# Kernel optimization log

Hardware: AMD Instinct MI355X
Metric: run time of the kernel (lower is better)

Reference implementation:

```python
import jax, jax.numpy as jnp
import numpy as np

HID = 3072
HEADS = 24
HD = HID // HEADS  # 128
MLP = 4 * HID      # 12288
B, L, TXT = 1, 2304, 256
EPS_LN = 1e-6
EPS_RMS = 1e-6


def setup_inputs() -> dict:
    key = jax.random.key(0)
    ks = jax.random.split(key, 12)
    s = 0.02
    return {
        "hidden_states": jax.random.normal(ks[0], (B, L, HID), jnp.float32),
        "temb": jax.random.normal(ks[1], (B, HID), jnp.float32),
        "cos": jax.random.normal(ks[2], (L - TXT, HD), jnp.float32),
        "sin": jax.random.normal(ks[3], (L - TXT, HD), jnp.float32),
        "ada_w": jax.random.normal(ks[4], (HID, 3 * HID), jnp.float32) * s,
        "ada_b": jnp.zeros((3 * HID,), jnp.float32),
        "lin1_w": jax.random.normal(ks[5], (HID, 3 * HID + MLP), jnp.float32) * s,
        "lin1_b": jnp.zeros((3 * HID + MLP,), jnp.float32),
        "lin2_w": jax.random.normal(ks[6], (HID + MLP, HID), jnp.float32) * s,
        "lin2_b": jnp.zeros((HID,), jnp.float32),
        "qn_w": jnp.ones((HD,), jnp.float32),
        "kn_w": jnp.ones((HD,), jnp.float32),
        "txt_len": TXT,
    }


def _rotate_half(x):
    # interleaved pairs: (x0,x1) -> (-x1, x0)
    xr = x[..., 0::2]
    xi = x[..., 1::2]
    return jnp.stack([-xi, xr], axis=-1).reshape(x.shape)


def _rms_norm(x, w):
    var = jnp.mean(jnp.square(x), axis=-1, keepdims=True)
    return x * jax.lax.rsqrt(var + EPS_RMS) * w


def reference(hidden_states, temb, cos, sin, ada_w, ada_b, lin1_w, lin1_b,
              lin2_w, lin2_b, qn_w, kn_w, txt_len):
    # AdaLayerNormZeroSingle
    emb = jax.nn.silu(temb) @ ada_w + ada_b               # [B, 3*HID]
    shift, scale, gate = jnp.split(emb, 3, axis=-1)
    mu = jnp.mean(hidden_states, axis=-1, keepdims=True)
    var = jnp.var(hidden_states, axis=-1, keepdims=True)
    ln = (hidden_states - mu) * jax.lax.rsqrt(var + EPS_LN)
    norm_x = ln * (1.0 + scale[:, None, :]) + shift[:, None, :]

    # fused qkv + mlp-in projection
    proj = norm_x @ lin1_w + lin1_b                       # [B, L, 3*HID+MLP]
    qkv, mlp = proj[..., : 3 * HID], proj[..., 3 * HID:]
    qkv = qkv.reshape(B, L, 3, HEADS, HD)
    q, k, v = qkv[:, :, 0], qkv[:, :, 1], qkv[:, :, 2]    # [B, L, H, D]

    q = _rms_norm(q, qn_w)
    k = _rms_norm(k, kn_w)

    # RoPE on image tokens only (first L - txt_len)
    img = L - txt_len
    c = cos[None, :, None, :]
    s = sin[None, :, None, :]
    q_img = q[:, :img] * c + _rotate_half(q[:, :img]) * s
    k_img = k[:, :img] * c + _rotate_half(k[:, :img]) * s
    q = jnp.concatenate([q_img, q[:, img:]], axis=1)
    k = jnp.concatenate([k_img, k[:, img:]], axis=1)

    # SDPA (full, non-causal)
    scale_a = 1.0 / jnp.sqrt(jnp.asarray(HD, q.dtype))
    scores = jnp.einsum("blhd,bmhd->bhlm", q, k) * scale_a
    probs = jax.nn.softmax(scores, axis=-1)
    attn = jnp.einsum("bhlm,bmhd->blhd", probs, v).reshape(B, L, HID)

    # gated parallel-MLP output
    out = jnp.concatenate([attn, jax.nn.gelu(mlp, approximate=True)], axis=-1)
    out = out @ lin2_w + lin2_b
    return hidden_states + out * gate[:, None, :]
```

## Files before the change

kernel.cpp:

```cpp
#include <hip/hip_runtime.h>
#include <stdint.h>

#define HID   3072
#define LSEQ  2304
#define NH    24
#define HD    128
#define N1    21504
#define QKVW  9216
#define X2W   15360

typedef __bf16 bf16x8 __attribute__((ext_vector_type(8)));
typedef unsigned short u16x8 __attribute__((ext_vector_type(8)));
typedef float f32x4 __attribute__((ext_vector_type(4)));

#define MFMA(a,b,c) __builtin_amdgcn_mfma_f32_16x16x32_bf16((a),(b),(c),0,0,0)

#define GLOAD_LDS16(g, l) __builtin_amdgcn_global_load_lds( \
    (const __attribute__((address_space(1))) unsigned int*)(g), \
    (__attribute__((address_space(3))) unsigned int*)(l), 16, 0, 0)

__device__ __forceinline__ unsigned short f2b(float f){
  unsigned int u = __builtin_bit_cast(unsigned int, f);
  u += 0x7fffu + ((u >> 16) & 1u);
  return (unsigned short)(u >> 16);
}
__device__ __forceinline__ float b2f(unsigned short b){
  return __builtin_bit_cast(float, ((unsigned int)b) << 16);
}
__device__ __forceinline__ unsigned int pk2(float lo, float hi){
  return (unsigned int)f2b(lo) | ((unsigned int)f2b(hi) << 16);
}

__global__ void silu_k(const float* __restrict__ temb, float* __restrict__ st){
  int i = blockIdx.x*256 + threadIdx.x;
  if (i < HID){ float x = temb[i]; st[i] = x / (1.f + __expf(-x)); }
}

__global__ __launch_bounds__(256) void ada_k(const float* __restrict__ st,
                                             const float* __restrict__ aw,
                                             const float* __restrict__ ab,
                                             float* __restrict__ emb){
  int c = threadIdx.x & 31, g = threadIdx.x >> 5;
  int col = blockIdx.x*32 + c;
  float acc = 0.f;
  for (int k = g; k < HID; k += 8)
    acc += st[k] * aw[(size_t)k*QKVW + col];
  __shared__ float part[256];
  part[threadIdx.x] = acc;
  __syncthreads();
  if (threadIdx.x < 32){
    float s = 0.f;
    #pragma unroll
    for (int j = 0; j < 8; ++j) s += part[j*32 + threadIdx.x];
    int cc = blockIdx.x*32 + threadIdx.x;
    emb[cc] = s + ab[cc];
  }
}

__global__ __launch_bounds__(256) void ln_k(const float* __restrict__ hs,
                                            const float* __restrict__ emb,
                                            unsigned short* __restrict__ nx){
  int l = blockIdx.x, t = threadIdx.x;
  const float* row = hs + (size_t)l*HID;
  float x[12], s = 0.f, ss = 0.f;
  #pragma unroll
  for (int i = 0; i < 12; ++i){ x[i] = row[t + i*256]; s += x[i]; ss += x[i]*x[i]; }
  #pragma unroll
  for (int off = 32; off; off >>= 1){ s += __shfl_xor(s, off); ss += __shfl_xor(ss, off); }
  __shared__ float red[8];
  int w = t >> 6, lane = t & 63;
  if (!lane){ red[w] = s; red[4+w] = ss; }
  __syncthreads();
  s = red[0]+red[1]+red[2]+red[3];
  ss = red[4]+red[5]+red[6]+red[7];
  float mu = s * (1.f/HID);
  float var = ss * (1.f/HID) - mu*mu;
  float rstd = rsqrtf(var + 1e-6f);
  #pragma unroll
  for (int i = 0; i < 12; ++i){
    int c = t + i*256;
    float v = (x[i]-mu)*rstd*(1.f + emb[HID + c]) + emb[c];
    nx[(size_t)l*HID + c] = f2b(v);
  }
}

__global__ __launch_bounds__(256) void tconv_k(const float* __restrict__ W,
                                               unsigned short* __restrict__ WT,
                                               int ldw, int K){
  __shared__ unsigned short Ls[64*66];
  int k0 = blockIdx.x*64, n0 = blockIdx.y*64;
  int t = threadIdx.x;
  #pragma unroll
  for (int p = 0; p < 4; ++p){
    int idx = p*256 + t, row = idx >> 4, c4 = idx & 15;
    float4 f = *(const float4*)(W + (size_t)(k0+row)*ldw + n0 + c4*4);
    *(unsigned int*)&Ls[row*66 + c4*4]     = pk2(f.x, f.y);
    *(unsigned int*)&Ls[row*66 + c4*4 + 2] = pk2(f.z, f.w);
  }
  __syncthreads();
  #pragma unroll
  for (int p = 0; p < 2; ++p){
    int idx = p*256 + t, n = idx >> 3, ch = idx & 7;
    u16x8 r;
    #pragma unroll
    for (int j = 0; j < 8; ++j) r[j] = Ls[(ch*8 + j)*66 + n];
    *(uint4*)(WT + (size_t)(n0+n)*K + k0 + ch*8) = __builtin_bit_cast(uint4, r);
  }
}

template<int EPI>
__global__ __launch_bounds__(512, 2)
void gemm256_k(const unsigned short* __restrict__ A, const unsigned short* __restrict__ BT,
               const float* __restrict__ bias, int K, int NT,
               unsigned short* __restrict__ o16)
{
  __shared__ __align__(16) unsigned short As[4][256*32];
  __shared__ __align__(16) unsigned short Bs[4][256*32];
  const int t = threadIdx.x;
  const int m0 = blockIdx.y * 256, n0 = blockIdx.x * 256;
  const int w = t >> 6, lane = t & 63, quad = lane >> 4, l16 = lane & 15;
  const int wr = w >> 2, wc = w & 3;

  const unsigned short* aSrc[2];
  const unsigned short* bSrc[2];
  #pragma unroll
  for (int p = 0; p < 2; ++p){
    int lin = p*512 + t;
    int row = lin >> 2;
    int ch  = (lin & 3) ^ ((row >> 1) & 3);
    aSrc[p] = A  + (size_t)(m0 + row)*K + ch*8;
    bSrc[p] = BT + (size_t)(n0 + row)*K + ch*8;
  }
  const int ldsOff0 = w*512;
  const int ldsOff1 = 4096 + w*512;

#define STAGE_A(slot, pf) do{ \
    GLOAD_LDS16(aSrc[0] + (size_t)(pf)*32, &As[slot][ldsOff0]); \
    GLOAD_LDS16(aSrc[1] + (size_t)(pf)*32, &As[slot][ldsOff1]); }while(0)
#define STAGE_B(slot, pf) do{ \
    GLOAD_LDS16(bSrc[0] + (size_t)(pf)*32, &Bs[slot][ldsOff0]); \
    GLOAD_LDS16(bSrc[1] + (size_t)(pf)*32, &Bs[slot][ldsOff1]); }while(0)

  const int kSwz  = (quad ^ ((l16 >> 1) & 3)) * 8;
  const int aBase = (wr*128 + l16)*32 + kSwz;
  const int bBase = (wc*64  + l16)*32 + kSwz;

  f32x4 acc[8][4];
  #pragma unroll
  for (int i = 0; i < 8; ++i)
    #pragma unroll
    for (int j = 0; j < 4; ++j) acc[i][j] = (f32x4){0.f,0.f,0.f,0.f};

  STAGE_A(0, 0); STAGE_B(0, 0);
  STAGE_A(1, 1); STAGE_B(1, 1);
  STAGE_A(2, 2); STAGE_B(2, 2);
  asm volatile("s_waitcnt vmcnt(8)" ::: "memory");
  __builtin_amdgcn_sched_barrier(0);
  __builtin_amdgcn_s_barrier();

  for (int kt = 0; kt < NT; ++kt){
    const int slot  = kt & 3;
    const int wslot = (kt + 3) & 3;
    const int pf    = (kt + 3 < NT) ? (kt + 3) : (NT - 1);
    bf16x8 af[4], bf[4];

    STAGE_A(wslot, pf);
    #pragma unroll
    for (int i = 0; i < 4; ++i)
      af[i] = __builtin_bit_cast(bf16x8, *(const uint4*)&As[slot][aBase + i*512]);
    #pragma unroll
    for (int i = 0; i < 4; ++i)
      bf[i] = __builtin_bit_cast(bf16x8, *(const uint4*)&Bs[slot][bBase + i*512]);
    __builtin_amdgcn_s_barrier();
    asm volatile("s_waitcnt lgkmcnt(0)" ::: "memory");
    __builtin_amdgcn_sched_barrier(0);
    __builtin_amdgcn_s_setprio(1);
    #pragma unroll
    for (int mi = 0; mi < 4; ++mi)
      #pragma unroll
      for (int ni = 0; ni < 4; ++ni)
        acc[mi][ni] = MFMA(af[mi], bf[ni], acc[mi][ni]);
    __builtin_amdgcn_s_setprio(0);

    STAGE_B(wslot, pf);
    #pragma unroll
    for (int i = 0; i < 4; ++i)
      af[i] = __builtin_bit_cast(bf16x8, *(const uint4*)&As[slot][aBase + 2048 + i*512]);
    __builtin_amdgcn_s_barrier();
    asm volatile("s_waitcnt lgkmcnt(0)" ::: "memory");
    __builtin_amdgcn_sched_barrier(0);
    __builtin_amdgcn_s_setprio(1);
    #pragma unroll
    for (int mi = 0; mi < 4; ++mi)
      #pragma unroll
      for (int ni = 0; ni < 4; ++ni)
        acc[4+mi][ni] = MFMA(af[mi], bf[ni], acc[4+mi][ni]);
    __builtin_amdgcn_s_setprio(0);
    asm volatile("s_waitcnt vmcnt(8)" ::: "memory");
    __builtin_amdgcn_sched_barrier(0);
    __builtin_amdgcn_s_barrier();
  }
#undef STAGE_A
#undef STAGE_B

  asm volatile("s_waitcnt vmcnt(0)" ::: "memory");

  #pragma unroll
  for (int mi = 0; mi < 8; ++mi){
    #pragma unroll
    for (int ni = 0; ni < 4; ++ni){
      const int gn = n0 + wc*64 + ni*16 + l16;
      const float bs = bias[gn];
      #pragma unroll
      for (int r = 0; r < 4; ++r){
        const int gm = m0 + wr*128 + mi*16 + quad*4 + r;
        float v = acc[mi][ni][r] + bs;
        if (EPI == 1){
          o16[(size_t)gm*QKVW + gn] = f2b(v);
        } else {
          float e = __expf(1.5957691216057308f*(v + 0.044715f*v*v*v));
          float th = 1.f - 2.f/(e + 1.f);
          o16[(size_t)gm*X2W + HID + gn] = f2b(0.5f*v*(1.f + th));
        }
      }
    }
  }
}

template<int EPI>
__global__ __launch_bounds__(256)
void gemm_k(const unsigned short* __restrict__ A, const unsigned short* __restrict__ BT,
            const float* __restrict__ bias, int K,
            unsigned short* __restrict__ o16, float* __restrict__ of,
            const float* __restrict__ hid, const float* __restrict__ emb)
{
  __shared__ __align__(16) unsigned short As[128*32];
  __shared__ __align__(16) unsigned short Bs[128*32];
  const int t = threadIdx.x;
  const int m0 = blockIdx.y * 128, n0 = blockIdx.x * 128;
  const int w = t >> 6, lane = t & 63, quad = lane >> 4, l16 = lane & 15;
  const int wm = w >> 1, wn = w & 1;

  f32x4 acc[4][4];
  #pragma unroll
  for (int i = 0; i < 4; ++i)
    #pragma unroll
    for (int j = 0; j < 4; ++j) acc[i][j] = (f32x4){0.f,0.f,0.f,0.f};

  const unsigned short* aG = A  + (size_t)(m0 + w*32 + (lane>>2))*K + (lane&3)*8;
  const unsigned short* bG = BT + (size_t)(n0 + w*32 + (lane>>2))*K + (lane&3)*8;
  unsigned short* aL = &As[w*1024];
  unsigned short* bL = &Bs[w*1024];

  for (int k0 = 0; k0 < K; k0 += 32){
    __syncthreads();
    GLOAD_LDS16(aG + k0,          aL);
    GLOAD_LDS16(aG + 16*K + k0,   aL + 512);
    GLOAD_LDS16(bG + k0,          bL);
    GLOAD_LDS16(bG + 16*K + k0,   bL + 512);
    __syncthreads();

    bf16x8 af[4], bf[4];
    #pragma unroll
    for (int mt = 0; mt < 4; ++mt)
      af[mt] = __builtin_bit_cast(bf16x8, *(const uint4*)&As[(wm*64 + mt*16 + l16)*32 + quad*8]);
    #pragma unroll
    for (int nt = 0; nt < 4; ++nt)
      bf[nt] = __builtin_bit_cast(bf16x8, *(const uint4*)&Bs[(wn*64 + nt*16 + l16)*32 + quad*8]);
    #pragma unroll
    for (int mt = 0; mt < 4; ++mt)
      #pragma unroll
      for (int nt = 0; nt < 4; ++nt)
        acc[mt][nt] = MFMA(af[mt], bf[nt], acc[mt][nt]);
  }

  #pragma unroll
  for (int mt = 0; mt < 4; ++mt){
    #pragma unroll
    for (int nt = 0; nt < 4; ++nt){
      const int gn = n0 + wn*64 + nt*16 + l16;
      const float bs = bias[gn];
      #pragma unroll
      for (int r = 0; r < 4; ++r){
        const int gm = m0 + wm*64 + mt*16 + quad*4 + r;
        float v = acc[mt][nt][r] + bs;
        if (EPI == 1){
          o16[(size_t)gm*QKVW + gn] = f2b(v);
        } else if (EPI == 3){
          float e = __expf(1.5957691216057308f*(v + 0.044715f*v*v*v));
          float th = 1.f - 2.f/(e + 1.f);
          o16[(size_t)gm*X2W + HID + gn] = f2b(0.5f*v*(1.f + th));
        } else {
          of[(size_t)gm*HID + gn] = hid[(size_t)gm*HID + gn] + v * emb[2*HID + gn];
        }
      }
    }
  }
}

__global__ __launch_bounds__(256) void qknorm_k(unsigned short* __restrict__ qkv,
                                                const float* __restrict__ qn,
                                                const float* __restrict__ kn,
                                                const float* __restrict__ cosp,
                                                const float* __restrict__ sinp,
                                                const int* __restrict__ txtp){
  int img = LSEQ - txtp[0];
  int rid = blockIdx.x*4 + (threadIdx.x >> 6);
  int lane = threadIdx.x & 63;
  int which = rid / (NH*LSEQ);
  int rem   = rid % (NH*LSEQ);
  int h = rem / LSEQ, l = rem % LSEQ;
  unsigned short* p = qkv + (size_t)l*QKVW + which*HID + h*HD + lane*2;
  unsigned int both = *(const unsigned int*)p;
  float x0 = b2f((unsigned short)(both & 0xffffu));
  float x1 = b2f((unsigned short)(both >> 16));
  float ss = x0*x0 + x1*x1;
  #pragma unroll
  for (int off = 32; off; off >>= 1) ss += __shfl_xor(ss, off);
  float r = rsqrtf(ss*(1.f/HD) + 1e-6f);
  const float* wv = which ? kn : qn;
  float y0 = x0*r*wv[lane*2], y1 = x1*r*wv[lane*2+1];
  if (l < img){
    float c0 = cosp[l*HD + lane*2], c1 = cosp[l*HD + lane*2 + 1];
    float s0 = sinp[l*HD + lane*2], s1 = sinp[l*HD + lane*2 + 1];
    float t0 = y0*c0 - y1*s0;
    float t1 = y1*c1 + y0*s1;
    y0 = t0; y1 = t1;
  }
  if (which == 0){ y0 *= 0.08838834764831845f; y1 *= 0.08838834764831845f; }
  *(unsigned int*)p = pk2(y0, y1);
}

__global__ __launch_bounds__(256) void vtrans_k(const unsigned short* __restrict__ qkv,
                                                unsigned short* __restrict__ vT){
  __shared__ __align__(16) unsigned short Ls[64*136];
  int h = blockIdx.y, m0 = blockIdx.x*64, t = threadIdx.x;
  #pragma unroll
  for (int p = 0; p < 4; ++p){
    int lin = p*256 + t, m = lin >> 4, ch = lin & 15;
    *(uint4*)&Ls[m*136 + ch*8] =
      *(const uint4*)(qkv + (size_t)(m0+m)*QKVW + 2*HID + h*HD + ch*8);
  }
  __syncthreads();
  #pragma unroll
  for (int p = 0; p < 4; ++p){
    int lin = p*256 + t, d = lin >> 3, ch = lin & 7;
    u16x8 r;
    #pragma unroll
    for (int j = 0; j < 8; ++j) r[j] = Ls[(ch*8 + j)*136 + d];
    *(uint4*)(vT + (size_t)h*HD*LSEQ + (size_t)d*LSEQ + m0 + ch*8) =
      __builtin_bit_cast(uint4, r);
  }
}

__global__ __launch_bounds__(256)
void attn_k(const unsigned short* __restrict__ qkv,
            const unsigned short* __restrict__ vT,
            unsigned short* __restrict__ x2)
{
  __shared__ __align__(16) unsigned short Ks[32*136];
  __shared__ __align__(16) unsigned short Vt[128*40];
  __shared__ __align__(16) unsigned short Ps[4*16*40];
  const int h = blockIdx.y, qb = blockIdx.x*64;
  const int t = threadIdx.x, w = t >> 6, lane = t & 63, quad = lane >> 4, l16 = lane & 15;

  bf16x8 aq[4];
  {
    const unsigned short* qp = qkv + (size_t)(qb + w*16 + l16)*QKVW + h*HD;
    #pragma unroll
    for (int dt = 0; dt < 4; ++dt)
      aq[dt] = __builtin_bit_cast(bf16x8, *(const uint4*)(qp + dt*32 + quad*8));
  }
  f32x4 o[8];
  #pragma unroll
  for (int i = 0; i < 8; ++i) o[i] = (f32x4){0.f,0.f,0.f,0.f};
  float mr[4] = {-1e30f,-1e30f,-1e30f,-1e30f};
  float lr[4] = {0.f,0.f,0.f,0.f};

  const unsigned short* kb = qkv + HID + h*HD;
  const unsigned short* vb = vT + (size_t)h*HD*LSEQ;
  unsigned short* pw = &Ps[w*16*40];

  for (int m0 = 0; m0 < LSEQ; m0 += 32){
    __syncthreads();
    #pragma unroll
    for (int p = 0; p < 2; ++p){
      int lin = p*256 + t, kr = lin >> 4, ch = lin & 15;
      *(uint4*)&Ks[kr*136 + ch*8] = *(const uint4*)(kb + (size_t)(m0+kr)*QKVW + ch*8);
    }
    #pragma unroll
    for (int p = 0; p < 2; ++p){
      int lin = p*256 + t, d = lin >> 2, ch = lin & 3;
      *(uint4*)&Vt[d*40 + ch*8] = *(const uint4*)(vb + (size_t)d*LSEQ + m0 + ch*8);
    }
    __syncthreads();

    f32x4 s0 = (f32x4){0.f,0.f,0.f,0.f}, s1 = s0;
    #pragma unroll
    for (int dt = 0; dt < 4; ++dt){
      bf16x8 k0 = __builtin_bit_cast(bf16x8, *(const uint4*)&Ks[l16*136 + dt*32 + quad*8]);
      bf16x8 k1 = __builtin_bit_cast(bf16x8, *(const uint4*)&Ks[(16+l16)*136 + dt*32 + quad*8]);
      s0 = MFMA(aq[dt], k0, s0);
      s1 = MFMA(aq[dt], k1, s1);
    }
    #pragma unroll
    for (int r = 0; r < 4; ++r){
      float mx = fmaxf(s0[r], s1[r]);
      mx = fmaxf(mx, __shfl_xor(mx, 1));
      mx = fmaxf(mx, __shfl_xor(mx, 2));
      mx = fmaxf(mx, __shfl_xor(mx, 4));
      mx = fmaxf(mx, __shfl_xor(mx, 8));
      float mn = fmaxf(mr[r], mx);
      float al = __expf(mr[r] - mn);
      float p0 = __expf(s0[r] - mn), p1 = __expf(s1[r] - mn);
      float rs = p0 + p1;
      rs += __shfl_xor(rs, 1);
      rs += __shfl_xor(rs, 2);
      rs += __shfl_xor(rs, 4);
      rs += __shfl_xor(rs, 8);
      lr[r] = lr[r]*al + rs;
      mr[r] = mn;
      #pragma unroll
      for (int i = 0; i < 8; ++i) o[i][r] *= al;
      int q = quad*4 + r;
      pw[q*40 + l16]      = f2b(p0);
      pw[q*40 + 16 + l16] = f2b(p1);
    }
    bf16x8 pa = __builtin_bit_cast(bf16x8, *(const uint4*)&pw[l16*40 + quad*8]);
    #pragma unroll
    for (int i = 0; i < 8; ++i){
      bf16x8 vv = __builtin_bit_cast(bf16x8, *(const uint4*)&Vt[(i*16 + l16)*40 + quad*8]);
      o[i] = MFMA(pa, vv, o[i]);
    }
  }
  #pragma unroll
  for (int i = 0; i < 8; ++i){
    #pragma unroll
    for (int r = 0; r < 4; ++r){
      int q = qb + w*16 + quad*4 + r;
      x2[(size_t)q*X2W + h*HD + i*16 + l16] = f2b(o[i][r] / lr[r]);
    }
  }
}

extern "C" void kernel_launch(void* const* d_in, const int* in_sizes, int n_in,
                              void* d_out, int out_size, void* d_ws, size_t ws_size,
                              hipStream_t stream) {
  const float* hs     = (const float*)d_in[0];
  const float* temb   = (const float*)d_in[1];
  const float* cosp   = (const float*)d_in[2];
  const float* sinp   = (const float*)d_in[3];
  const float* ada_w  = (const float*)d_in[4];
  const float* ada_b  = (const float*)d_in[5];
  const float* lin1_w = (const float*)d_in[6];
  const float* lin1_b = (const float*)d_in[7];
  const float* lin2_w = (const float*)d_in[8];
  const float* lin2_b = (const float*)d_in[9];
  const float* qn     = (const float*)d_in[10];
  const float* kn     = (const float*)d_in[11];
  const int*   txt    = (const int*)d_in[12];
  float* out = (float*)d_out;

  char* ws = (char*)d_ws;
  float*          st  = (float*)ws;
  float*          emb = (float*)(ws + 12288);
  unsigned short* nx  = (unsigned short*)(ws + 49152);
  unsigned short* qkv = (unsigned short*)(ws + 14204928);
  unsigned short* x2  = (unsigned short*)(ws + 56672256);
  unsigned short* vT  = (unsigned short*)(ws + 127451136);
  unsigned short* wt  = (unsigned short*)(ws + 141606912);

  silu_k<<<12, 256, 0, stream>>>(temb, st);
  ada_k<<<288, 256, 0, stream>>>(st, ada_w, ada_b, emb);
  ln_k<<<LSEQ, 256, 0, stream>>>(hs, emb, nx);

  tconv_k<<<dim3(HID/64, QKVW/64), 256, 0, stream>>>(lin1_w, wt, N1, HID);
  gemm256_k<1><<<dim3(QKVW/256, LSEQ/256), 512, 0, stream>>>(nx, wt, lin1_b, HID, HID/32, qkv);
  tconv_k<<<dim3(HID/64, (N1-QKVW)/64), 256, 0, stream>>>(lin1_w + QKVW, wt, N1, HID);
  gemm256_k<3><<<dim3((N1-QKVW)/256, LSEQ/256), 512, 0, stream>>>(nx, wt, lin1_b + QKVW, HID, HID/32, x2);

  qknorm_k<<<(2*NH*LSEQ)/4, 256, 0, stream>>>(qkv, qn, kn, cosp, sinp, txt);
  vtrans_k<<<dim3(LSEQ/64, NH), 256, 0, stream>>>(qkv, vT);
  attn_k<<<dim3(LSEQ/64, NH), 256, 0, stream>>>(qkv, vT, x2);

  tconv_k<<<dim3(X2W/64, HID/64), 256, 0, stream>>>(lin2_w, wt, HID, X2W);
  gemm_k<2><<<dim3(HID/128, LSEQ/128), 256, 0, stream>>>(x2, wt, lin2_b, X2W,
                                                         nullptr, out, hs, emb);
}
```

Measured before the change: 1.901 ms.

## Replace lin2 GEMM with 4-stage pipelined 128x256 tile kernel; add MFMA priority in attention

```diff
diff --git a/kernel.cpp b/kernel.cpp
--- a/kernel.cpp
+++ b/kernel.cpp
@@ -227,19 +227,39 @@
   }
 }
 
-template<int EPI>
-__global__ __launch_bounds__(256)
-void gemm_k(const unsigned short* __restrict__ A, const unsigned short* __restrict__ BT,
-            const float* __restrict__ bias, int K,
-            unsigned short* __restrict__ o16, float* __restrict__ of,
-            const float* __restrict__ hid, const float* __restrict__ emb)
+__global__ __launch_bounds__(512, 2)
+void gemm256n_k(const unsigned short* __restrict__ A, const unsigned short* __restrict__ BT,
+                const float* __restrict__ bias, int K, int NT,
+                float* __restrict__ of, const float* __restrict__ hid,
+                const float* __restrict__ emb)
 {
-  __shared__ __align__(16) unsigned short As[128*32];
-  __shared__ __align__(16) unsigned short Bs[128*32];
+  __shared__ __align__(16) unsigned short As[4][128*32];
+  __shared__ __align__(16) unsigned short Bs[4][256*32];
   const int t = threadIdx.x;
-  const int m0 = blockIdx.y * 128, n0 = blockIdx.x * 128;
+  const int m0 = blockIdx.y * 128, n0 = blockIdx.x * 256;
   const int w = t >> 6, lane = t & 63, quad = lane >> 4, l16 = lane & 15;
-  const int wm = w >> 1, wn = w & 1;
+  const int wr = w >> 2, wc = w & 3;
+
+  const unsigned short* aSrc;
+  { int row = t >> 2, ch = (t & 3) ^ ((row >> 1) & 3);
+    aSrc = A + (size_t)(m0 + row)*K + ch*8; }
+  const unsigned short* bSrc[2];
+  #pragma unroll
+  for (int p = 0; p < 2; ++p){
+    int lin = p*512 + t, row = lin >> 2, ch = (lin & 3) ^ ((row >> 1) & 3);
+    bSrc[p] = BT + (size_t)(n0 + row)*K + ch*8;
+  }
+  const int aOff  = w*512;
+  const int bOff0 = w*512, bOff1 = 4096 + w*512;
+
+#define STAGE(slot, pf) do{ \
+    GLOAD_LDS16(aSrc    + (size_t)(pf)*32, &As[slot][aOff]); \
+    GLOAD_LDS16(bSrc[0] + (size_t)(pf)*32, &Bs[slot][bOff0]); \
+    GLOAD_LDS16(bSrc[1] + (size_t)(pf)*32, &Bs[slot][bOff1]); }while(0)
+
+  const int kSwz  = (quad ^ ((l16 >> 1) & 3)) * 8;
+  const int aBase = (wr*64 + l16)*32 + kSwz;
+  const int bBase = (wc*64 + l16)*32 + kSwz;
 
   f32x4 acc[4][4];
   #pragma unroll
@@ -247,52 +267,53 @@
     #pragma unroll
     for (int j = 0; j < 4; ++j) acc[i][j] = (f32x4){0.f,0.f,0.f,0.f};
 
-  const unsigned short* aG = A  + (size_t)(m0 + w*32 + (lane>>2))*K + (lane&3)*8;
-  const unsigned short* bG = BT + (size_t)(n0 + w*32 + (lane>>2))*K + (lane&3)*8;
-  unsigned short* aL = &As[w*1024];
-  unsigned short* bL = &Bs[w*1024];
-
-  for (int k0 = 0; k0 < K; k0 += 32){
-    __syncthreads();
-    GLOAD_LDS16(aG + k0,          aL);
-    GLOAD_LDS16(aG + 16*K + k0,   aL + 512);
-    GLOAD_LDS16(bG + k0,          bL);
-    GLOAD_LDS16(bG + 16*K + k0,   bL + 512);
-    __syncthreads();
-
+  STAGE(0, 0); STAGE(1, 1); STAGE(2, 2);
+  asm volatile("s_waitcnt vmcnt(6)" ::: "memory");
+  __builtin_amdgcn_sched_barrier(0);
+  __builtin_amdgcn_s_barrier();
+
+  for (int kt = 0; kt < NT; ++kt){
+    const int slot  = kt & 3;
+    const int wslot = (kt + 3) & 3;
+    const int pf    = (kt + 3 < NT) ? (kt + 3) : (NT - 1);
     bf16x8 af[4], bf[4];
-    #pragma unroll
-    for (int mt = 0; mt < 4; ++mt)
-      af[mt] = __builtin_bit_cast(bf16x8, *(const uint4*)&As[(wm*64 + mt*16 + l16)*32 + quad*8]);
-    #pragma unroll
-    for (int nt = 0; nt < 4; ++nt)
-      bf[nt] = __builtin_bit_cast(bf16x8, *(const uint4*)&Bs[(wn*64 + nt*16 + l16)*32 + quad*8]);
-    #pragma unroll
-    for (int mt = 0; mt < 4; ++mt)
+
+    STAGE(wslot, pf);
+    #pragma unroll
+    for (int i = 0; i < 4; ++i)
+      af[i] = __builtin_bit_cast(bf16x8, *(const uint4*)&As[slot][aBase + i*512]);
+    #pragma unroll
+    for (int i = 0; i < 4; ++i)
+      bf[i] = __builtin_bit_cast(bf16x8, *(const uint4*)&Bs[slot][bBase + i*512]);
+    __builtin_amdgcn_s_barrier();
+    asm volatile("s_waitcnt lgkmcnt(0)" ::: "memory");
+    __builtin_amdgcn_sched_barrier(0);
+    __builtin_amdgcn_s_setprio(1);
+    #pragma unroll
+    for (int mi = 0; mi < 4; ++mi)
       #pragma unroll
-      for (int nt = 0; nt < 4; ++nt)
-        acc[mt][nt] = MFMA(af[mt], bf[nt], acc[mt][nt]);
-  }
-
-  #pragma unroll
-  for (int mt = 0; mt < 4; ++mt){
-    #pragma unroll
-    for (int nt = 0; nt < 4; ++nt){
-      const int gn = n0 + wn*64 + nt*16 + l16;
+      for (int ni = 0; ni < 4; ++ni)
+        acc[mi][ni] = MFMA(af[mi], bf[ni], acc[mi][ni]);
+    __builtin_amdgcn_s_setprio(0);
+    asm volatile("s_waitcnt vmcnt(6)" ::: "memory");
+    __builtin_amdgcn_sched_barrier(0);
+    __builtin_amdgcn_s_barrier();
+  }
+#undef STAGE
+
+  asm volatile("s_waitcnt vmcnt(0)" ::: "memory");
+
+  #pragma unroll
+  for (int mi = 0; mi < 4; ++mi){
+    #pragma unroll
+    for (int ni = 0; ni < 4; ++ni){
+      const int gn = n0 + wc*64 + ni*16 + l16;
       const float bs = bias[gn];
       #pragma unroll
       for (int r = 0; r < 4; ++r){
-        const int gm = m0 + wm*64 + mt*16 + quad*4 + r;
-        float v = acc[mt][nt][r] + bs;
-        if (EPI == 1){
-          o16[(size_t)gm*QKVW + gn] = f2b(v);
-        } else if (EPI == 3){
-          float e = __expf(1.5957691216057308f*(v + 0.044715f*v*v*v));
-          float th = 1.f - 2.f/(e + 1.f);
-          o16[(size_t)gm*X2W + HID + gn] = f2b(0.5f*v*(1.f + th));
-        } else {
-          of[(size_t)gm*HID + gn] = hid[(size_t)gm*HID + gn] + v * emb[2*HID + gn];
-        }
+        const int gm = m0 + wr*64 + mi*16 + quad*4 + r;
+        float v = acc[mi][ni][r] + bs;
+        of[(size_t)gm*HID + gn] = hid[(size_t)gm*HID + gn] + v * emb[2*HID + gn];
       }
     }
   }
@@ -396,6 +417,7 @@
     __syncthreads();
 
     f32x4 s0 = (f32x4){0.f,0.f,0.f,0.f}, s1 = s0;
+    __builtin_amdgcn_s_setprio(1);
     #pragma unroll
     for (int dt = 0; dt < 4; ++dt){
       bf16x8 k0 = __builtin_bit_cast(bf16x8, *(const uint4*)&Ks[l16*136 + dt*32 + quad*8]);
@@ -403,6 +425,7 @@
       s0 = MFMA(aq[dt], k0, s0);
       s1 = MFMA(aq[dt], k1, s1);
     }
+    __builtin_amdgcn_s_setprio(0);
     #pragma unroll
     for (int r = 0; r < 4; ++r){
       float mx = fmaxf(s0[r], s1[r]);
@@ -427,11 +450,13 @@
       pw[q*40 + 16 + l16] = f2b(p1);
     }
     bf16x8 pa = __builtin_bit_cast(bf16x8, *(const uint4*)&pw[l16*40 + quad*8]);
+    __builtin_amdgcn_s_setprio(1);
     #pragma unroll
     for (int i = 0; i < 8; ++i){
       bf16x8 vv = __builtin_bit_cast(bf16x8, *(const uint4*)&Vt[(i*16 + l16)*40 + quad*8]);
       o[i] = MFMA(pa, vv, o[i]);
     }
+    __builtin_amdgcn_s_setprio(0);
   }
   #pragma unroll
   for (int i = 0; i < 8; ++i){
@@ -484,6 +509,6 @@
   attn_k<<<dim3(LSEQ/64, NH), 256, 0, stream>>>(qkv, vT, x2);
 
   tconv_k<<<dim3(X2W/64, HID/64), 256, 0, stream>>>(lin2_w, wt, HID, X2W);
-  gemm_k<2><<<dim3(HID/128, LSEQ/128), 256, 0, stream>>>(x2, wt, lin2_b, X2W,
-                                                         nullptr, out, hs, emb);
-}
+  gemm256n_k<<<dim3(HID/256, LSEQ/128), 512, 0, stream>>>(x2, wt, lin2_b, X2W, X2W/32,
+                                                          out, hs, emb);
+}
```

Result: no change. 1.917 ms (+0.9%).
